# Kernel optimization log

Measured on AMD Instinct MI355X. Metric: run time of the kernel, lower is better.

The kernel has to match this reference:

```python
import jax, jax.numpy as jnp
import numpy as np

B, S, D = 4, 2048, 1024
H = 4096          # d_model * hidden_mult
E = 8             # n_experts
TOP_K = 2
AUX_COEF = 0.01


def setup_inputs() -> dict:
    key = jax.random.key(0)
    ks = jax.random.split(key, 5)
    x = jax.random.normal(ks[0], (B, S, D), dtype=jnp.float32)
    router_w = jax.random.normal(ks[1], (D, E), dtype=jnp.float32) * 0.02
    temp = jnp.ones((1,), dtype=jnp.float32)
    Wg = jax.random.normal(ks[2], (E, D, H), dtype=jnp.float32) * 0.02
    Wu = jax.random.normal(ks[3], (E, D, H), dtype=jnp.float32) * 0.02
    Wd = jax.random.normal(ks[4], (E, H, D), dtype=jnp.float32) * 0.02
    return {"x": x, "router_w": router_w, "temp": temp, "Wg": Wg, "Wu": Wu, "Wd": Wd}


def reference(x, router_w, temp, Wg, Wu, Wd):
    # --- Top2Router (eval mode: no jitter noise, no dropout) ---
    t = jnp.clip(temp, 0.1, 5.0)                         # scalar temp param, clamped
    logits = jnp.einsum('bsd,de->bse', x, router_w) / t   # [B,S,E]
    probs = jax.nn.softmax(logits, axis=-1)
    w, idx = jax.lax.top_k(probs, TOP_K)                  # [B,S,K] weights / expert ids

    # --- Expert dispatch / compute / combine ---
    # dropless=True -> no capacity dropping. Tokens not routed to expert e get
    # combine weight 0, so a masked-weight dense accumulate matches the
    # gather->MLP->scatter math of the original exactly.
    out = jnp.zeros_like(x)
    for e in range(E):  # fixed small expert count; structurally distinct weights
        we = jnp.sum(w * (idx == e), axis=-1)             # [B,S] combine weight for expert e
        gate = jnp.einsum('bsd,dh->bsh', x, Wg[e])
        up = jnp.einsum('bsd,dh->bsh', x, Wu[e])
        hidden = jax.nn.silu(up) * gate                   # swiglu: silu(up_proj) * gate_proj
        ye = jnp.einsum('bsh,hd->bsd', hidden, Wd[e])
        out = out + we[..., None] * ye

    # --- Aux losses ---
    importance = probs.mean(axis=(0, 1))                  # [E]
    assigned = jnp.sum(jax.nn.one_hot(idx, E, dtype=probs.dtype), axis=(0, 1, 2))  # [E]
    load = assigned / (B * S + 1e-6)
    aux_load_loss = (importance * load).sum() * E * AUX_COEF
    router_entropy = -(probs * jnp.log(jnp.clip(probs, 1e-8))).sum(-1).mean() * 0.01
    overflow_pct = jnp.zeros((), dtype=x.dtype)           # dropless -> never overflows
    return out, aux_load_loss, router_entropy, overflow_pct
```

## Files before the change

### kernel.cpp

```cpp
#include <hip/hip_runtime.h>
#include <stdint.h>

#define T_TOK 8192
#define D_DIM 1024
#define H_DIM 4096
#define NGU   8192
#define NEXP  8
#define MAX_YT 136

typedef float  f32x4  __attribute__((ext_vector_type(4)));
typedef __bf16 bf16x8 __attribute__((ext_vector_type(8)));
typedef __bf16 bf16x4 __attribute__((ext_vector_type(4)));

__device__ __forceinline__ void gl_lds16(const void* g, void* l) {
  __builtin_amdgcn_global_load_lds(
      (__attribute__((address_space(1))) void*)g,
      (__attribute__((address_space(3))) void*)l, 16u, 0, 0u);
}

__global__ __launch_bounds__(256) void router_kernel(
    const float* __restrict__ x, const float* __restrict__ rw,
    const float* __restrict__ temp, __bf16* __restrict__ xb,
    int* __restrict__ rowtok, float* __restrict__ rowwt,
    int* __restrict__ cnt, float* __restrict__ imp_part,
    float* __restrict__ ent_part)
{
  const int wid  = threadIdx.x >> 6;
  const int lane = threadIdx.x & 63;
  const int t    = blockIdx.x * 4 + wid;

  float acc[8];
#pragma unroll
  for (int e = 0; e < 8; e++) acc[e] = 0.f;
  const float* xr = x + (size_t)t * D_DIM;
#pragma unroll
  for (int it = 0; it < 4; it++) {
    int d = (it * 64 + lane) * 4;
    float4 v = *(const float4*)(xr + d);
    bf16x4 o;
    o[0] = (__bf16)v.x; o[1] = (__bf16)v.y;
    o[2] = (__bf16)v.z; o[3] = (__bf16)v.w;
    *(bf16x4*)(xb + (size_t)t * D_DIM + d) = o;
    float vv[4] = {v.x, v.y, v.z, v.w};
#pragma unroll
    for (int j = 0; j < 4; j++) {
      float xv = vv[j];
      const float4 r0 = *(const float4*)(rw + (d + j) * 8);
      const float4 r1 = *(const float4*)(rw + (d + j) * 8 + 4);
      acc[0] += xv * r0.x; acc[1] += xv * r0.y;
      acc[2] += xv * r0.z; acc[3] += xv * r0.w;
      acc[4] += xv * r1.x; acc[5] += xv * r1.y;
      acc[6] += xv * r1.z; acc[7] += xv * r1.w;
    }
  }
#pragma unroll
  for (int e = 0; e < 8; e++) {
    float v = acc[e];
#pragma unroll
    for (int off = 32; off > 0; off >>= 1) v += __shfl_xor(v, off, 64);
    acc[e] = v;
  }
  float tclamp = fminf(fmaxf(temp[0], 0.1f), 5.0f);
  float invt = 1.0f / tclamp;
  float mx = -1e30f;
#pragma unroll
  for (int e = 0; e < 8; e++) { acc[e] *= invt; mx = fmaxf(mx, acc[e]); }
  float p[8]; float s = 0.f;
#pragma unroll
  for (int e = 0; e < 8; e++) { p[e] = __expf(acc[e] - mx); s += p[e]; }
  float invs = 1.0f / s;
  float ent = 0.f;
#pragma unroll
  for (int e = 0; e < 8; e++) {
    p[e] *= invs;
    ent -= p[e] * __logf(fmaxf(p[e], 1e-8f));
  }
  int i1 = 0; float w1 = p[0];
#pragma unroll
  for (int e = 1; e < 8; e++) if (p[e] > w1) { w1 = p[e]; i1 = e; }
  int i2 = (i1 == 0) ? 1 : 0; float w2 = p[i2];
#pragma unroll
  for (int e = 0; e < 8; e++) if (e != i1 && p[e] > w2) { w2 = p[e]; i2 = e; }

  __shared__ float s_imp[4][8];
  __shared__ float s_ent[4];
  if (lane == 0) {
    int pos1 = atomicAdd(&cnt[i1], 1);
    rowtok[i1 * T_TOK + pos1] = t * 2;
    rowwt [i1 * T_TOK + pos1] = w1;
    int pos2 = atomicAdd(&cnt[i2], 1);
    rowtok[i2 * T_TOK + pos2] = t * 2 + 1;
    rowwt [i2 * T_TOK + pos2] = w2;
#pragma unroll
    for (int e = 0; e < 8; e++) s_imp[wid][e] = p[e];
    s_ent[wid] = ent;
  }
  __syncthreads();
  if (threadIdx.x < 8) {
    int e = threadIdx.x;
    imp_part[blockIdx.x * 8 + e] =
        s_imp[0][e] + s_imp[1][e] + s_imp[2][e] + s_imp[3][e];
  } else if (threadIdx.x == 8) {
    ent_part[blockIdx.x] = s_ent[0] + s_ent[1] + s_ent[2] + s_ent[3];
  }
}

__global__ __launch_bounds__(256) void aux_final_kernel(
    const float* __restrict__ imp_part, const float* __restrict__ ent_part,
    const int* __restrict__ cnt, int* __restrict__ tileoff,
    float* __restrict__ out_aux)
{
  __shared__ float simp[256];
  __shared__ float sent[256];
  int tid = threadIdx.x;
  int e = tid & 7, g = tid >> 3;
  float ia = 0.f;
  for (int b = g; b < 2048; b += 32) ia += imp_part[b * 8 + e];
  simp[tid] = ia;
  float ea = 0.f;
  for (int b = tid; b < 2048; b += 256) ea += ent_part[b];
  sent[tid] = ea;
  __syncthreads();
  if (tid == 0) {
    float imp[8] = {0,0,0,0,0,0,0,0};
    float ent = 0.f;
    for (int i = 0; i < 256; i++) { imp[i & 7] += simp[i]; ent += sent[i]; }
    float aux = 0.f;
    for (int ee = 0; ee < 8; ee++) {
      float importance = imp[ee] / 8192.0f;
      float load = (float)cnt[ee] / (8192.0f + 1e-6f);
      aux += importance * load;
    }
    out_aux[0] = aux * 8.0f * 0.01f;
    out_aux[1] = (ent / 8192.0f) * 0.01f;
    out_aux[2] = 0.f;
    int off = 0;
    for (int ee = 0; ee < 8; ee++) { tileoff[ee] = off; off += (cnt[ee] + 127) >> 7; }
    tileoff[8] = off;
  }
}

__global__ __launch_bounds__(256) void transpose_all_kernel(
    const float* __restrict__ Wg, const float* __restrict__ Wu,
    const float* __restrict__ Wd,
    __bf16* __restrict__ BguT, __bf16* __restrict__ BdT)
{
  __shared__ float tile[64 * 129];
  int z = blockIdx.z;
  const float* src; __bf16* dst;
  int C, Kd, r0, c0, up = 0;
  bool gu = z < 16;
  if (gu) {
    int e = z >> 1; up = z & 1;
    src = (up ? Wu : Wg) + (size_t)e * D_DIM * H_DIM;
    dst = BguT + (size_t)e * NGU * D_DIM;
    C = H_DIM; Kd = D_DIM;
    c0 = (blockIdx.x & 31) << 7;  r0 = (blockIdx.x >> 5) << 6;
  } else {
    int e = z - 16;
    src = Wd + (size_t)e * H_DIM * D_DIM;
    dst = BdT + (size_t)e * D_DIM * H_DIM;
    C = D_DIM; Kd = H_DIM;
    c0 = (blockIdx.x & 7) << 7;   r0 = (blockIdx.x >> 3) << 6;
  }
  int t = threadIdx.x;
  int cq = t & 31, rb = t >> 5;
#pragma unroll
  for (int i = 0; i < 8; i++) {
    int r = rb + 8 * i;
    float4 v = *(const float4*)(src + (size_t)(r0 + r) * C + c0 + cq * 4);
    *(float4*)&tile[r * 129 + cq * 4] = v;
  }
  __syncthreads();
#pragma unroll
  for (int i = 0; i < 4; i++) {
    int c = t + (i << 8);
    int hl = c >> 3;
    int rc = c & 7;
    int dstrow;
    if (gu) { int h = c0 + hl; dstrow = ((h >> 4) << 5) + (h & 15) + (up << 4); }
    else    { dstrow = c0 + hl; }
    bf16x8 o;
#pragma unroll
    for (int j = 0; j < 8; j++)
      o[j] = (__bf16)tile[(rc * 8 + j) * 129 + hl];
    *(bf16x8*)(dst + (size_t)dstrow * Kd + r0 + rc * 8) = o;
  }
}

__global__ __launch_bounds__(256, 2) void gemm1_kernel(
    const __bf16* __restrict__ xb, const __bf16* __restrict__ BguT,
    const int* __restrict__ rowtok, const float* __restrict__ rowwt,
    const int* __restrict__ cnt, const int* __restrict__ tileoff,
    __bf16* __restrict__ hid)
{
  __shared__ __bf16 As[128 * 64];
  __shared__ __bf16 Bs[128 * 64];
  __shared__ int   s_tok[128];
  __shared__ float s_wt[128];

  const int nblk8 = (64 * MAX_YT) >> 3;
  int hwlin = blockIdx.y * 64 + blockIdx.x;
  int lin = (hwlin & 7) * nblk8 + (hwlin >> 3);
  int y  = lin >> 6;
  int bx = lin & 63;

  if (y >= tileoff[8]) return;
  int e = 0;
  while (y >= tileoff[e + 1]) e++;
  int m0 = (y - tileoff[e]) << 7;
  int cntE = cnt[e];
  int tid = threadIdx.x;
  if (tid < 128) {
    int m = m0 + tid;
    bool v = m < cntE;
    s_tok[tid] = v ? rowtok[e * T_TOK + m] : 0;
    s_wt [tid] = v ? rowwt [e * T_TOK + m] : 0.f;
  }
  __syncthreads();

  const int n0 = bx << 7;
  const __bf16* Bp = BguT + (size_t)e * NGU * D_DIM;
  const int lane = tid & 63;
  const int wid = tid >> 6;
  const int wm = wid >> 1, wn = wid & 1;
  const int l15 = lane & 15, l4 = lane >> 4;

  f32x4 zero = {0.f, 0.f, 0.f, 0.f};
  f32x4 acc[4][4];
#pragma unroll
  for (int a = 0; a < 4; a++)
#pragma unroll
    for (int b = 0; b < 4; b++) acc[a][b] = zero;

  int q[4], ar[4], akc[4];
#pragma unroll
  for (int c = 0; c < 4; c++) {
    q[c]   = tid + (c << 8);
    ar[c]  = q[c] >> 3;
    akc[c] = ((q[c] & 7) ^ (ar[c] & 7)) << 3;
  }

  for (int kt = 0; kt < 16; kt++) {
    int k0 = kt << 6;
#pragma unroll
    for (int c = 0; c < 4; c++) {
      const __bf16* ga = xb + (size_t)(s_tok[ar[c]] >> 1) * D_DIM + (k0 + akc[c]);
      gl_lds16(ga, &As[q[c] << 3]);
    }
#pragma unroll
    for (int c = 0; c < 4; c++) {
      const __bf16* gb = Bp + (size_t)(n0 + ar[c]) * D_DIM + (k0 + akc[c]);
      gl_lds16(gb, &Bs[q[c] << 3]);
    }
    __syncthreads();
#pragma unroll
    for (int ks = 0; ks < 2; ks++) {
      bf16x8 af[4], bfv[4];
#pragma unroll
      for (int mi = 0; mi < 4; mi++) {
        int row = wm * 64 + mi * 16 + l15;
        int kidx = (ks * 4 + l4) ^ (row & 7);
        af[mi] = *(const bf16x8*)&As[(row * 8 + kidx) * 8];
      }
#pragma unroll
      for (int ni = 0; ni < 4; ni++) {
        int row = wn * 64 + ni * 16 + l15;
        int kidx = (ks * 4 + l4) ^ (row & 7);
        bfv[ni] = *(const bf16x8*)&Bs[(row * 8 + kidx) * 8];
      }
#pragma unroll
      for (int mi = 0; mi < 4; mi++)
#pragma unroll
        for (int ni = 0; ni < 4; ni++)
          acc[mi][ni] = __builtin_amdgcn_mfma_f32_16x16x32_bf16(
              af[mi], bfv[ni], acc[mi][ni], 0, 0, 0);
    }
    __syncthreads();
  }

#pragma unroll
  for (int mi = 0; mi < 4; mi++) {
#pragma unroll
    for (int p2 = 0; p2 < 2; p2++) {
      f32x4 gt = acc[mi][2 * p2];
      f32x4 up = acc[mi][2 * p2 + 1];
      int nb = n0 + wn * 64 + p2 * 32;
      int h = ((nb >> 5) << 4) + l15;
#pragma unroll
      for (int r = 0; r < 4; r++) {
        int rl = wm * 64 + mi * 16 + l4 * 4 + r;
        if (m0 + rl < cntE) {
          float u = up[r];
          float hv = (u / (1.f + __expf(-u))) * gt[r] * s_wt[rl];
          hid[(size_t)s_tok[rl] * H_DIM + h] = (__bf16)hv;
        }
      }
    }
  }
}

__global__ __launch_bounds__(256, 2) void gemm2_kernel(
    const __bf16* __restrict__ hid, const __bf16* __restrict__ BdT,
    const int* __restrict__ rowtok, const int* __restrict__ cnt,
    const int* __restrict__ tileoff, float* __restrict__ out)
{
  __shared__ __bf16 As[128 * 64];
  __shared__ __bf16 Bs[128 * 64];
  __shared__ int s_tok[128];

  const int nblk8 = (8 * MAX_YT) >> 3;
  int hwlin = blockIdx.y * 8 + blockIdx.x;
  int lin = (hwlin & 7) * nblk8 + (hwlin >> 3);
  int y  = lin >> 3;
  int bx = lin & 7;

  if (y >= tileoff[8]) return;
  int e = 0;
  while (y >= tileoff[e + 1]) e++;
  int m0 = (y - tileoff[e]) << 7;
  int cntE = cnt[e];
  int tid = threadIdx.x;
  if (tid < 128) {
    int m = m0 + tid;
    s_tok[tid] = (m < cntE) ? rowtok[e * T_TOK + m] : 0;
  }
  __syncthreads();

  const int n0 = bx << 7;
  const __bf16* Bp = BdT + (size_t)e * D_DIM * H_DIM;
  const int lane = tid & 63;
  const int wid = tid >> 6;
  const int wm = wid >> 1, wn = wid & 1;
  const int l15 = lane & 15, l4 = lane >> 4;

  f32x4 zero = {0.f, 0.f, 0.f, 0.f};
  f32x4 acc[4][4];
#pragma unroll
  for (int a = 0; a < 4; a++)
#pragma unroll
    for (int b = 0; b < 4; b++) acc[a][b] = zero;

  int q[4], ar[4], akc[4];
#pragma unroll
  for (int c = 0; c < 4; c++) {
    q[c]   = tid + (c << 8);
    ar[c]  = q[c] >> 3;
    akc[c] = ((q[c] & 7) ^ (ar[c] & 7)) << 3;
  }

  for (int kt = 0; kt < 64; kt++) {
    int k0 = kt << 6;
#pragma unroll
    for (int c = 0; c < 4; c++) {
      const __bf16* ga = hid + (size_t)s_tok[ar[c]] * H_DIM + (k0 + akc[c]);
      gl_lds16(ga, &As[q[c] << 3]);
    }
#pragma unroll
    for (int c = 0; c < 4; c++) {
      const __bf16* gb = Bp + (size_t)(n0 + ar[c]) * H_DIM + (k0 + akc[c]);
      gl_lds16(gb, &Bs[q[c] << 3]);
    }
    __syncthreads();
#pragma unroll
    for (int ks = 0; ks < 2; ks++) {
      bf16x8 af[4], bfv[4];
#pragma unroll
      for (int mi = 0; mi < 4; mi++) {
        int row = wm * 64 + mi * 16 + l15;
        int kidx = (ks * 4 + l4) ^ (row & 7);
        af[mi] = *(const bf16x8*)&As[(row * 8 + kidx) * 8];
      }
#pragma unroll
      for (int ni = 0; ni < 4; ni++) {
        int row = wn * 64 + ni * 16 + l15;
        int kidx = (ks * 4 + l4) ^ (row & 7);
        bfv[ni] = *(const bf16x8*)&Bs[(row * 8 + kidx) * 8];
      }
#pragma unroll
      for (int mi = 0; mi < 4; mi++)
#pragma unroll
        for (int ni = 0; ni < 4; ni++)
          acc[mi][ni] = __builtin_amdgcn_mfma_f32_16x16x32_bf16(
              af[mi], bfv[ni], acc[mi][ni], 0, 0, 0);
    }
    __syncthreads();
  }

#pragma unroll
  for (int mi = 0; mi < 4; mi++)
#pragma unroll
    for (int ni = 0; ni < 4; ni++) {
      int coln = n0 + wn * 64 + ni * 16 + l15;
#pragma unroll
      for (int r = 0; r < 4; r++) {
        int rl = wm * 64 + mi * 16 + l4 * 4 + r;
        if (m0 + rl < cntE)
          atomicAdd(&out[(size_t)(s_tok[rl] >> 1) * D_DIM + coln],
                    acc[mi][ni][r]);
      }
    }
}

extern "C" void kernel_launch(void* const* d_in, const int* in_sizes, int n_in,
                              void* d_out, int out_size, void* d_ws, size_t ws_size,
                              hipStream_t stream)
{
  const float* x    = (const float*)d_in[0];
  const float* rw   = (const float*)d_in[1];
  const float* temp = (const float*)d_in[2];
  const float* Wg   = (const float*)d_in[3];
  const float* Wu   = (const float*)d_in[4];
  const float* Wd   = (const float*)d_in[5];
  float* out = (float*)d_out;

  char* ws = (char*)d_ws;
  size_t off = 0;
  auto alloc = [&](size_t bytes) -> void* {
    void* p = ws + off;
    off = (off + bytes + 255) & ~(size_t)255;
    return p;
  };
  __bf16* xb     = (__bf16*)alloc((size_t)T_TOK * D_DIM * 2);
  __bf16* BguT   = (__bf16*)alloc((size_t)NEXP * NGU * D_DIM * 2);
  __bf16* BdT    = (__bf16*)alloc((size_t)NEXP * D_DIM * H_DIM * 2);
  __bf16* hid    = (__bf16*)alloc((size_t)T_TOK * 2 * H_DIM * 2);
  int*    rowtok = (int*)  alloc((size_t)NEXP * T_TOK * 4);
  float*  rowwt  = (float*)alloc((size_t)NEXP * T_TOK * 4);
  int*    cnt    = (int*)  alloc(64);
  int*    tileoff= (int*)  alloc(64);
  float*  imp_part = (float*)alloc(2048 * 8 * 4);
  float*  ent_part = (float*)alloc(2048 * 4);
  (void)ws_size; (void)n_in; (void)in_sizes;

  hipMemsetAsync(cnt, 0, 64, stream);
  hipMemsetAsync(out, 0, (size_t)T_TOK * D_DIM * sizeof(float), stream);

  router_kernel<<<2048, 256, 0, stream>>>(x, rw, temp, xb, rowtok, rowwt, cnt,
                                          imp_part, ent_part);
  aux_final_kernel<<<1, 256, 0, stream>>>(imp_part, ent_part, cnt, tileoff,
                                          out + (size_t)T_TOK * D_DIM);
  transpose_all_kernel<<<dim3(512, 1, 24), 256, 0, stream>>>(Wg, Wu, Wd,
                                                             BguT, BdT);
  gemm1_kernel<<<dim3(64, MAX_YT), 256, 0, stream>>>(xb, BguT, rowtok, rowwt,
                                                     cnt, tileoff, hid);
  gemm2_kernel<<<dim3(8, MAX_YT), 256, 0, stream>>>(hid, BdT, rowtok, cnt,
                                                    tileoff, out);
}
```

Measured before the change: 1.168 ms.

## Load weight fragments directly from global into registers, drop B LDS staging

Both expert GEMMs now read B-operand (weight) fragments straight from global memory into registers in MFMA layout, and no longer stage them through shared memory. This halves the LDS footprint and removes the LDS B reads. The XCD-aware block-index remapping is also dropped in favour of a plain blockIdx mapping. The trade-offs are that each wave pair now loads the weights redundantly, with less coalesced 16-byte loads, and that the global load latency is exposed inside the k-loop with no prefetch. Losing the swizzle may also hurt L2 locality.

```diff
diff --git a/kernel.cpp b/kernel.cpp
--- a/kernel.cpp
+++ b/kernel.cpp
@@ -195,16 +195,10 @@
     __bf16* __restrict__ hid)
 {
   __shared__ __bf16 As[128 * 64];
-  __shared__ __bf16 Bs[128 * 64];
   __shared__ int   s_tok[128];
   __shared__ float s_wt[128];
 
-  const int nblk8 = (64 * MAX_YT) >> 3;
-  int hwlin = blockIdx.y * 64 + blockIdx.x;
-  int lin = (hwlin & 7) * nblk8 + (hwlin >> 3);
-  int y  = lin >> 6;
-  int bx = lin & 63;
-
+  int y = blockIdx.y;
   if (y >= tileoff[8]) return;
   int e = 0;
   while (y >= tileoff[e + 1]) e++;
@@ -219,7 +213,7 @@
   }
   __syncthreads();
 
-  const int n0 = bx << 7;
+  const int n0 = blockIdx.x << 7;
   const __bf16* Bp = BguT + (size_t)e * NGU * D_DIM;
   const int lane = tid & 63;
   const int wid = tid >> 6;
@@ -240,6 +234,7 @@
     ar[c]  = q[c] >> 3;
     akc[c] = ((q[c] & 7) ^ (ar[c] & 7)) << 3;
   }
+  const __bf16* bbase = Bp + (size_t)(n0 + wn * 64 + l15) * D_DIM + l4 * 8;
 
   for (int kt = 0; kt < 16; kt++) {
     int k0 = kt << 6;
@@ -248,15 +243,17 @@
       const __bf16* ga = xb + (size_t)(s_tok[ar[c]] >> 1) * D_DIM + (k0 + akc[c]);
       gl_lds16(ga, &As[q[c] << 3]);
     }
-#pragma unroll
-    for (int c = 0; c < 4; c++) {
-      const __bf16* gb = Bp + (size_t)(n0 + ar[c]) * D_DIM + (k0 + akc[c]);
-      gl_lds16(gb, &Bs[q[c] << 3]);
-    }
+    bf16x8 bfv[2][4];
+#pragma unroll
+    for (int ks = 0; ks < 2; ks++)
+#pragma unroll
+      for (int ni = 0; ni < 4; ni++)
+        bfv[ks][ni] = *(const bf16x8*)&bbase[(size_t)(ni * 16) * D_DIM +
+                                             k0 + ks * 32];
     __syncthreads();
 #pragma unroll
     for (int ks = 0; ks < 2; ks++) {
-      bf16x8 af[4], bfv[4];
+      bf16x8 af[4];
 #pragma unroll
       for (int mi = 0; mi < 4; mi++) {
         int row = wm * 64 + mi * 16 + l15;
@@ -264,17 +261,11 @@
         af[mi] = *(const bf16x8*)&As[(row * 8 + kidx) * 8];
       }
 #pragma unroll
-      for (int ni = 0; ni < 4; ni++) {
-        int row = wn * 64 + ni * 16 + l15;
-        int kidx = (ks * 4 + l4) ^ (row & 7);
-        bfv[ni] = *(const bf16x8*)&Bs[(row * 8 + kidx) * 8];
-      }
-#pragma unroll
       for (int mi = 0; mi < 4; mi++)
 #pragma unroll
         for (int ni = 0; ni < 4; ni++)
           acc[mi][ni] = __builtin_amdgcn_mfma_f32_16x16x32_bf16(
-              af[mi], bfv[ni], acc[mi][ni], 0, 0, 0);
+              af[mi], bfv[ks][ni], acc[mi][ni], 0, 0, 0);
     }
     __syncthreads();
   }
@@ -306,15 +297,9 @@
     const int* __restrict__ tileoff, float* __restrict__ out)
 {
   __shared__ __bf16 As[128 * 64];
-  __shared__ __bf16 Bs[128 * 64];
   __shared__ int s_tok[128];
 
-  const int nblk8 = (8 * MAX_YT) >> 3;
-  int hwlin = blockIdx.y * 8 + blockIdx.x;
-  int lin = (hwlin & 7) * nblk8 + (hwlin >> 3);
-  int y  = lin >> 3;
-  int bx = lin & 7;
-
+  int y = blockIdx.y;
   if (y >= tileoff[8]) return;
   int e = 0;
   while (y >= tileoff[e + 1]) e++;
@@ -327,7 +312,7 @@
   }
   __syncthreads();
 
-  const int n0 = bx << 7;
+  const int n0 = blockIdx.x << 7;
   const __bf16* Bp = BdT + (size_t)e * D_DIM * H_DIM;
   const int lane = tid & 63;
   const int wid = tid >> 6;
@@ -348,6 +333,7 @@
     ar[c]  = q[c] >> 3;
     akc[c] = ((q[c] & 7) ^ (ar[c] & 7)) << 3;
   }
+  const __bf16* bbase = Bp + (size_t)(n0 + wn * 64 + l15) * H_DIM + l4 * 8;
 
   for (int kt = 0; kt < 64; kt++) {
     int k0 = kt << 6;
@@ -356,15 +342,17 @@
       const __bf16* ga = hid + (size_t)s_tok[ar[c]] * H_DIM + (k0 + akc[c]);
       gl_lds16(ga, &As[q[c] << 3]);
     }
-#pragma unroll
-    for (int c = 0; c < 4; c++) {
-      const __bf16* gb = Bp + (size_t)(n0 + ar[c]) * H_DIM + (k0 + akc[c]);
-      gl_lds16(gb, &Bs[q[c] << 3]);
-    }
+    bf16x8 bfv[2][4];
+#pragma unroll
+    for (int ks = 0; ks < 2; ks++)
+#pragma unroll
+      for (int ni = 0; ni < 4; ni++)
+        bfv[ks][ni] = *(const bf16x8*)&bbase[(size_t)(ni * 16) * H_DIM +
+                                             k0 + ks * 32];
     __syncthreads();
 #pragma unroll
     for (int ks = 0; ks < 2; ks++) {
-      bf16x8 af[4], bfv[4];
+      bf16x8 af[4];
 #pragma unroll
       for (int mi = 0; mi < 4; mi++) {
         int row = wm * 64 + mi * 16 + l15;
@@ -372,17 +360,11 @@
         af[mi] = *(const bf16x8*)&As[(row * 8 + kidx) * 8];
       }
 #pragma unroll
-      for (int ni = 0; ni < 4; ni++) {
-        int row = wn * 64 + ni * 16 + l15;
-        int kidx = (ks * 4 + l4) ^ (row & 7);
-        bfv[ni] = *(const bf16x8*)&Bs[(row * 8 + kidx) * 8];
-      }
-#pragma unroll
       for (int mi = 0; mi < 4; mi++)
 #pragma unroll
         for (int ni = 0; ni < 4; ni++)
           acc[mi][ni] = __builtin_amdgcn_mfma_f32_16x16x32_bf16(
-              af[mi], bfv[ni], acc[mi][ni], 0, 0, 0);
+              af[mi], bfv[ks][ni], acc[mi][ni], 0, 0, 0);
     }
     __syncthreads();
   }
```

Result: slower. 1.558 ms (+33.4%).
